# Kernel tuning notes

Measured on AMD Instinct MI355X. Metric: run time of the kernel, lower is better.

## Reference

```python
import jax, jax.numpy as jnp
import numpy as np

B, H = 16384, 64          # batch, human_num
SELF_DIM, HUMAN_DIM = 6, 7
D = 32                    # gcn2_w1_dim / embedding dim


def _lin(key, fin, fout):
    return jax.random.normal(key, (fin, fout), jnp.float32) / np.sqrt(fin)


def setup_inputs() -> dict:
    key = jax.random.key(0)
    ks = jax.random.split(key, 40)
    inp = {}
    inp["state"] = jax.random.normal(ks[0], (B, H, SELF_DIM + HUMAN_DIM), jnp.float32)
    inp["dropout"] = 0
    # w_r: mlp(6 -> 64 -> 32, last_relu=True)
    inp["wr_w1"] = _lin(ks[1], SELF_DIM, 64); inp["wr_b1"] = jnp.zeros(64, jnp.float32)
    inp["wr_w2"] = _lin(ks[2], 64, D);        inp["wr_b2"] = jnp.zeros(D, jnp.float32)
    # w_h: mlp(7 -> 64 -> 32, last_relu=True)
    inp["wh_w1"] = _lin(ks[3], HUMAN_DIM, 64); inp["wh_b1"] = jnp.zeros(64, jnp.float32)
    inp["wh_w2"] = _lin(ks[4], 64, D);         inp["wh_b2"] = jnp.zeros(D, jnp.float32)
    # hetero GraphConv weights: per edge type (rh: robot->human, hr: human->robot, hh: human->human),
    # per layer. GraphConv: out = lin_rel(scatter_sum(x_src)) + lin_root(x_dst); lin_root has no bias.
    i = 5
    for L in (1, 2):
        for et in ("rh", "hr", "hh"):
            inp[f"rel_{et}{L}"] = _lin(ks[i], D, D); i += 1
            inp[f"brel_{et}{L}"] = jnp.zeros(D, jnp.float32)
            inp[f"root_{et}{L}"] = _lin(ks[i], D, D); i += 1
    # value_net: mlp(32 -> 150 -> 100 -> 1), no last relu
    inp["vn_w1"] = _lin(ks[i], D, 150);  inp["vn_b1"] = jnp.zeros(150, jnp.float32); i += 1
    inp["vn_w2"] = _lin(ks[i], 150, 100); inp["vn_b2"] = jnp.zeros(100, jnp.float32); i += 1
    inp["vn_w3"] = _lin(ks[i], 100, 1);  inp["vn_b3"] = jnp.zeros(1, jnp.float32)
    return inp


def _hetero_layer(r, h, rel_rh, brel_rh, root_rh, rel_hr, brel_hr, root_hr,
                  rel_hh, brel_hh, root_hh):
    # r: [B, D] robot nodes; h: [B, H, D] human nodes
    sum_h = h.sum(axis=1)  # [B, D]
    # robot receives scatter-sum over all humans (star graph, one robot target)
    new_r = jax.nn.relu(sum_h @ rel_hr + brel_hr + r @ root_hr)
    # each human receives: robot message + sum of all OTHER humans (full graph minus self-loops)
    agg_hh = sum_h[:, None, :] - h  # [B, H, D]
    new_h = jax.nn.relu((r @ rel_rh)[:, None, :] + brel_rh
                        + agg_hh @ rel_hh + brel_hh
                        + h @ root_rh + h @ root_hh)
    return new_r, new_h


def _forward(state, wr_w1, wr_b1, wr_w2, wr_b2, wh_w1, wh_b1, wh_w2, wh_b2,
             rel_rh1, brel_rh1, root_rh1, rel_hr1, brel_hr1, root_hr1,
             rel_hh1, brel_hh1, root_hh1,
             rel_rh2, brel_rh2, root_rh2, rel_hr2, brel_hr2, root_hr2,
             rel_hh2, brel_hh2, root_hh2,
             vn_w1, vn_b1, vn_w2, vn_b2, vn_w3, vn_b3):
    self_state = state[:, 0, :SELF_DIM]        # [B, 6]
    human_states = state[:, :, SELF_DIM:]      # [B, H, 7]
    r = jax.nn.relu(jax.nn.relu(self_state @ wr_w1 + wr_b1) @ wr_w2 + wr_b2)      # [B, D]
    h = jax.nn.relu(jax.nn.relu(human_states @ wh_w1 + wh_b1) @ wh_w2 + wh_b2)    # [B, H, D]
    r, h = _hetero_layer(r, h, rel_rh1, brel_rh1, root_rh1, rel_hr1, brel_hr1,
                         root_hr1, rel_hh1, brel_hh1, root_hh1)
    r, h = _hetero_layer(r, h, rel_rh2, brel_rh2, root_rh2, rel_hr2, brel_hr2,
                         root_hr2, rel_hh2, brel_hh2, root_hh2)
    v = jax.nn.relu(r @ vn_w1 + vn_b1)
    v = jax.nn.relu(v @ vn_w2 + vn_b2)
    return v @ vn_w3 + vn_b3                    # [B, 1]


def reference(state, dropout, wr_w1, wr_b1, wr_w2, wr_b2, wh_w1, wh_b1, wh_w2, wh_b2,
              rel_rh1, brel_rh1, root_rh1, rel_hr1, brel_hr1, root_hr1,
              rel_hh1, brel_hh1, root_hh1,
              rel_rh2, brel_rh2, root_rh2, rel_hr2, brel_hr2, root_hr2,
              rel_hh2, brel_hh2, root_hh2,
              vn_w1, vn_b1, vn_w2, vn_b2, vn_w3, vn_b3):
    # dropout is accepted but unused (matches the torch forward signature)
    return _forward(state, wr_w1, wr_b1, wr_w2, wr_b2, wh_w1, wh_b1, wh_w2, wh_b2,
                    rel_rh1, brel_rh1, root_rh1, rel_hr1, brel_hr1, root_hr1,
                    rel_hh1, brel_hh1, root_hh1,
                    rel_rh2, brel_rh2, root_rh2, rel_hr2, brel_hr2, root_hr2,
                    rel_hh2, brel_hh2, root_hh2,
                    vn_w1, vn_b1, vn_w2, vn_b2, vn_w3, vn_b3)
```

## Files before the change

kernel.cpp:

```cpp
#include <hip/hip_runtime.h>

#define BTOT 16384

typedef __attribute__((ext_vector_type(8))) short bf16x8;
typedef __attribute__((ext_vector_type(4))) float f32x4;

#define MFMA16(a,b,c) __builtin_amdgcn_mfma_f32_16x16x32_bf16((a),(b),(c),0,0,0)

static __device__ __forceinline__ unsigned short bfhi(float x) {
    unsigned u = __float_as_uint(x);
    return (unsigned short)((u + 0x7FFFu + ((u >> 16) & 1u)) >> 16);
}
static __device__ __forceinline__ float b2f(unsigned short h) {
    return __uint_as_float(((unsigned)h) << 16);
}
static __device__ __forceinline__ unsigned short bflo(float x) {
    unsigned short h = bfhi(x);
    return bfhi(x - b2f(h));
}
static __device__ __forceinline__ unsigned pk2(float a, float b) {
    return (unsigned)bfhi(a) | ((unsigned)bfhi(b) << 16);
}
static __device__ __forceinline__ short f2s(float x) {
    return (short)bfhi(x);
}
static __device__ __forceinline__ bf16x8 zero8() {
    bf16x8 v;
    #pragma unroll
    for (int i = 0; i < 8; ++i) v[i] = 0;
    return v;
}

__global__ void pack_frags(
    const float* __restrict__ wh_w1, const float* __restrict__ wh_b1,
    const float* __restrict__ wh_w2,
    const float* __restrict__ root_rh1, const float* __restrict__ root_hh1,
    const float* __restrict__ rel_hh1,
    const float* __restrict__ wr_w2,
    const float* __restrict__ rel_hr1, const float* __restrict__ root_hr1,
    const float* __restrict__ rel_rh1,
    const float* __restrict__ rel_hr2, const float* __restrict__ root_hr2,
    const float* __restrict__ vn_w1, const float* __restrict__ vn_w2,
    const float* __restrict__ brel_hr1, const float* __restrict__ brel_rh1,
    const float* __restrict__ brel_hh1, const float* __restrict__ brel_hr2,
    short* __restrict__ pk)
{
    int t = blockIdx.x * blockDim.x + threadIdx.x;
    if (t < 52736) {
        int f = t >> 9, r = t & 511;
        int lane = r >> 3, j = r & 7;
        int q = lane >> 4, c = lane & 15;
        int k = q * 8 + j;
        unsigned short outv;
        if (f < 4) {
            int m = f * 16 + c;
            float v = (k < 7) ? wh_w1[k * 64 + m] : (k == 7 ? wh_b1[m] : 0.f);
            outv = bfhi(v);
        } else if (f < 8) {
            int u = f - 4, ks = u >> 1, nt = u & 1;
            outv = bfhi(wh_w2[(ks * 32 + k) * 32 + nt * 16 + c]);
        } else if (f < 10) {
            int n = (f - 8) * 16 + c;
            outv = bfhi(root_rh1[k * 32 + n] + root_hh1[k * 32 + n] - rel_hh1[k * 32 + n]);
        } else if (f < 22) {
            int u = f - 10, ks = u >> 1, nt = u & 1;
            int kp = ks * 32 + k;
            float w = wr_w2[(kp & 63) * 32 + nt * 16 + c];
            outv = (kp < 128) ? bfhi(w) : bflo(w);
        } else if (f < 46) {
            int u = f - 22, ks = u >> 2, nt = u & 3;
            int kp = ks * 32 + k, seg = kp >> 5, kk = kp & 31;
            int n2 = (nt & 1) * 16 + c;
            bool sPart = (seg < 2) || (seg == 4);
            const float* W = (nt < 2) ? (sPart ? rel_hr1 : root_hr1)
                                      : (sPart ? rel_hh1 : rel_rh1);
            float w = W[kk * 32 + n2];
            outv = (seg < 4) ? bfhi(w) : bflo(w);
        } else if (f < 58) {
            int u = f - 46, ks = u >> 1, nt = u & 1;
            int kp = ks * 32 + k, seg = kp >> 5, kk = kp & 31;
            int n = nt * 16 + c;
            bool sPart = (seg < 2) || (seg == 4);
            const float* W = sPart ? rel_hr2 : root_hr2;
            float w = W[kk * 32 + n];
            outv = (seg < 4) ? bfhi(w) : bflo(w);
        } else if (f < 68) {
            int n = (f - 58) * 16 + c;
            outv = (n < 150) ? bfhi(vn_w1[k * 150 + n]) : 0;
        } else {
            int u = f - 68, kt = u / 7, nt = u - kt * 7;
            int kk = kt * 32 + k, n = nt * 16 + c;
            outv = (kk < 150 && n < 100) ? bfhi(vn_w2[kk * 100 + n]) : 0;
        }
        pk[t] = (short)outv;
    } else if (t < 52800) {
        int i = t - 52736;
        float* bp = (float*)(pk + 52736);
        bp[i] = (i < 32) ? brel_hr1[i] : brel_rh1[i - 32] + brel_hh1[i - 32];
    } else if (t < 52832) {
        int i = t - 52800;
        float* bp = (float*)(pk + 52864);
        bp[i] = brel_hr2[i];
    }
}

__global__ __launch_bounds__(256) void fused_main(
    const float* __restrict__ state, const short* __restrict__ pk,
    const float* __restrict__ wr_w1, const float* __restrict__ wr_b1,
    const float* __restrict__ wr_b2, const float* __restrict__ wh_b2,
    short* __restrict__ r2buf)
{
    __shared__ short wbuf[4][4608];

    const int tid = threadIdx.x;
    const int wv = tid >> 6, lane = tid & 63;
    const int q = lane >> 4, c = lane & 15;
    const int b = blockIdx.x * 4 + wv;
    const float* st = state + (size_t)b * 832;
    short* T = wbuf[wv];

    const bf16x8* pk16 = (const bf16x8*)pk;
    const float* bg1f = (const float*)(pk + 52736);
    const float* bg2f = (const float*)(pk + 52864);
    const f32x4 z4 = {0.f, 0.f, 0.f, 0.f};

    bf16x8 A1[4], Bh2v[4], Bev[2];
    #pragma unroll
    for (int i = 0; i < 4; ++i) A1[i] = pk16[i * 64 + lane];
    #pragma unroll
    for (int i = 0; i < 4; ++i) Bh2v[i] = pk16[(4 + i) * 64 + lane];
    #pragma unroll
    for (int i = 0; i < 2; ++i) Bev[i] = pk16[(8 + i) * 64 + lane];

    {
        float hf[7];
        #pragma unroll
        for (int m = 0; m < 7; ++m) hf[m] = st[lane * 13 + 6 + m];
        uint4 v = make_uint4(pk2(hf[0], hf[1]), pk2(hf[2], hf[3]),
                             pk2(hf[4], hf[5]), pk2(hf[6], 1.0f));
        *(uint4*)(T + lane * 8) = v;
    }

    float trh;
    {
        float acc = wr_b1[lane];
        #pragma unroll
        for (int m = 0; m < 6; ++m) acc = fmaf(st[m], wr_w1[m * 64 + lane], acc);
        trh = fmaxf(acc, 0.f);
    }

    asm volatile("s_waitcnt lgkmcnt(0)" ::: "memory");

    bf16x8 bx[4];
    #pragma unroll
    for (int ht = 0; ht < 4; ++ht) {
        bf16x8 v = zero8();
        if (q == 0) v = *(const bf16x8*)(T + (ht * 16 + c) * 8);
        bx[ht] = v;
    }

    #pragma unroll
    for (int mh = 0; mh < 4; ++mh) {
        #pragma unroll
        for (int ht = 0; ht < 4; ++ht) {
            f32x4 d = MFMA16(A1[mh], bx[ht], z4);
            uint2 w = make_uint2(pk2(fmaxf(d[0], 0.f), fmaxf(d[1], 0.f)),
                                 pk2(fmaxf(d[2], 0.f), fmaxf(d[3], 0.f)));
            *(uint2*)(T + (ht * 16 + c) * 72 + mh * 16 + q * 4) = w;
        }
    }

    asm volatile("s_waitcnt lgkmcnt(0)" ::: "memory");

    const float b2a = wh_b2[c], b2b = wh_b2[16 + c];
    float ps0 = 0.f, ps1 = 0.f;
    #pragma unroll
    for (int mt = 0; mt < 4; ++mt) {
        bf16x8 a0 = *(const bf16x8*)(T + (mt * 16 + c) * 72 + q * 8);
        bf16x8 a1 = *(const bf16x8*)(T + (mt * 16 + c) * 72 + 32 + q * 8);
        f32x4 e0 = MFMA16(a0, Bh2v[0], z4); e0 = MFMA16(a1, Bh2v[2], e0);
        f32x4 e1 = MFMA16(a0, Bh2v[1], z4); e1 = MFMA16(a1, Bh2v[3], e1);
        #pragma unroll
        for (int r = 0; r < 4; ++r) {
            float v0 = fmaxf(e0[r] + b2a, 0.f), v1 = fmaxf(e1[r] + b2b, 0.f);
            int row = mt * 16 + q * 4 + r;
            T[row * 40 + c]      = f2s(v0);
            T[row * 40 + 16 + c] = f2s(v1);
            ps0 += v0; ps1 += v1;
        }
    }
    ps0 += __shfl_xor(ps0, 16); ps0 += __shfl_xor(ps0, 32);
    ps1 += __shfl_xor(ps1, 16); ps1 += __shfl_xor(ps1, 32);

    {
        short* SB = T + 2816;
        if (q == 0) {
            unsigned short h0 = bfhi(ps0), h1 = bfhi(ps1);
            SB[c] = (short)h0;        SB[16 + c] = (short)h1;
            SB[32 + c] = (short)bfhi(ps0 - b2f(h0));
            SB[48 + c] = (short)bfhi(ps1 - b2f(h1));
            SB[128 + c] = (short)h0;  SB[144 + c] = (short)h1;
        }
        short* TR = T + 3008;
        unsigned short th = bfhi(trh);
        TR[lane] = (short)th;
        TR[64 + lane] = (short)bfhi(trh - b2f(th));
        TR[128 + lane] = (short)th;
    }
    __syncthreads();

    if (wv == 0) {
        bf16x8 art[6];
        #pragma unroll
        for (int ks = 0; ks < 6; ++ks) {
            bf16x8 v = zero8();
            if (c < 4) v = *(const bf16x8*)(wbuf[c] + 3008 + ks * 32 + q * 8);
            art[ks] = v;
        }
        f32x4 dr0 = z4, dr1 = z4;
        #pragma unroll
        for (int ks = 0; ks < 6; ++ks) {
            dr0 = MFMA16(art[ks], pk16[(10 + ks * 2 + 0) * 64 + lane], dr0);
            dr1 = MFMA16(art[ks], pk16[(10 + ks * 2 + 1) * 64 + lane], dr1);
        }
        const float wb0 = wr_b2[c], wb1 = wr_b2[16 + c];
        if (q == 0) {
            #pragma unroll
            for (int r = 0; r < 4; ++r) {
                float v0 = fmaxf(dr0[r] + wb0, 0.f), v1 = fmaxf(dr1[r] + wb1, 0.f);
                short* SBr = wbuf[r] + 2816;
                unsigned short h0 = bfhi(v0), h1 = bfhi(v1);
                SBr[64 + c] = (short)h0;  SBr[96 + c]  = (short)bfhi(v0 - b2f(h0));  SBr[160 + c] = (short)h0;
                SBr[80 + c] = (short)h1;  SBr[112 + c] = (short)bfhi(v1 - b2f(h1));  SBr[176 + c] = (short)h1;
            }
        }
        asm volatile("s_waitcnt lgkmcnt(0)" ::: "memory");

        bf16x8 ag[6];
        #pragma unroll
        for (int ks = 0; ks < 6; ++ks) {
            bf16x8 v = zero8();
            if (c < 4) v = *(const bf16x8*)(wbuf[c] + 2816 + ks * 32 + q * 8);
            ag[ks] = v;
        }
        f32x4 dg[4] = {z4, z4, z4, z4};
        #pragma unroll
        for (int ks = 0; ks < 6; ++ks) {
            #pragma unroll
            for (int nt = 0; nt < 4; ++nt)
                dg[nt] = MFMA16(ag[ks], pk16[(22 + ks * 4 + nt) * 64 + lane], dg[nt]);
        }
        if (q == 0) {
            #pragma unroll
            for (int nt = 0; nt < 2; ++nt) {
                float bias = bg1f[nt * 16 + c];
                #pragma unroll
                for (int r = 0; r < 4; ++r) {
                    float v = fmaxf(dg[nt][r] + bias, 0.f);
                    short* G2r = wbuf[r] + 2624;
                    unsigned short hh = bfhi(v);
                    G2r[64 + nt * 16 + c]  = (short)hh;
                    G2r[96 + nt * 16 + c]  = (short)bfhi(v - b2f(hh));
                    G2r[160 + nt * 16 + c] = (short)hh;
                }
            }
            #pragma unroll
            for (int nt = 2; nt < 4; ++nt) {
                float bias = bg1f[nt * 16 + c];
                #pragma unroll
                for (int r = 0; r < 4; ++r)
                    ((float*)(wbuf[r] + 2560))[(nt - 2) * 16 + c] = dg[nt][r] + bias;
            }
        }
    }
    __syncthreads();

    {
        const float* C1 = (const float*)(T + 2560);
        const float c10 = C1[c], c11 = C1[16 + c];
        float t0 = 0.f, t1 = 0.f;
        #pragma unroll
        for (int mt = 0; mt < 4; ++mt) {
            bf16x8 ah = *(const bf16x8*)(T + (mt * 16 + c) * 40 + q * 8);
            f32x4 g0 = MFMA16(ah, Bev[0], z4);
            f32x4 g1 = MFMA16(ah, Bev[1], z4);
            #pragma unroll
            for (int r = 0; r < 4; ++r) {
                t0 += fmaxf(g0[r] + c10, 0.f);
                t1 += fmaxf(g1[r] + c11, 0.f);
            }
        }
        t0 += __shfl_xor(t0, 16); t0 += __shfl_xor(t0, 32);
        t1 += __shfl_xor(t1, 16); t1 += __shfl_xor(t1, 32);
        short* G2 = T + 2624;
        if (q == 0) {
            unsigned short h0 = bfhi(t0), h1 = bfhi(t1);
            G2[c] = (short)h0;        G2[16 + c] = (short)h1;
            G2[32 + c] = (short)bfhi(t0 - b2f(h0));
            G2[48 + c] = (short)bfhi(t1 - b2f(h1));
            G2[128 + c] = (short)h0;  G2[144 + c] = (short)h1;
        }
    }
    __syncthreads();

    if (wv == 0) {
        bf16x8 a2[6];
        #pragma unroll
        for (int ks = 0; ks < 6; ++ks) {
            bf16x8 v = zero8();
            if (c < 4) v = *(const bf16x8*)(wbuf[c] + 2624 + ks * 32 + q * 8);
            a2[ks] = v;
        }
        f32x4 d0 = z4, d1 = z4;
        #pragma unroll
        for (int ks = 0; ks < 6; ++ks) {
            d0 = MFMA16(a2[ks], pk16[(46 + ks * 2 + 0) * 64 + lane], d0);
            d1 = MFMA16(a2[ks], pk16[(46 + ks * 2 + 1) * 64 + lane], d1);
        }
        if (q == 0) {
            const int b0 = blockIdx.x * 4;
            const float g0 = bg2f[c], g1 = bg2f[16 + c];
            #pragma unroll
            for (int r = 0; r < 4; ++r) {
                r2buf[(b0 + r) * 32 + c]      = f2s(fmaxf(d0[r] + g0, 0.f));
                r2buf[(b0 + r) * 32 + 16 + c] = f2s(fmaxf(d1[r] + g1, 0.f));
            }
        }
    }
}

__global__ __launch_bounds__(256) void head_kernel(
    const short* __restrict__ pk,
    const float* __restrict__ vn_b1, const float* __restrict__ vn_b2,
    const float* __restrict__ vn_w3, const float* __restrict__ vn_b3,
    float* __restrict__ out)
{
    __shared__ __align__(16) short sh_v1[4][16 * 168];
    const int wv = threadIdx.x >> 6, lane = threadIdx.x & 63;
    const int q = lane >> 4, c = lane & 15;
    const int tile = blockIdx.x * 4 + wv;
    const bf16x8* wf = (const bf16x8*)pk;
    const short* r2b = pk + 53248;
    const f32x4 z4 = {0.f, 0.f, 0.f, 0.f};

    bf16x8 a1 = *(const bf16x8*)&r2b[(tile * 16 + c) * 32 + q * 8];
    short* vb = sh_v1[wv];
    #pragma unroll
    for (int nt = 0; nt < 10; ++nt) {
        f32x4 d = MFMA16(a1, wf[(58 + nt) * 64 + lane], z4);
        int n = nt * 16 + c;
        float bias = (n < 150) ? vn_b1[n] : 0.f;
        #pragma unroll
        for (int r = 0; r < 4; ++r) {
            float v = (n < 150) ? fmaxf(d[r] + bias, 0.f) : 0.f;
            vb[(q * 4 + r) * 168 + n] = f2s(v);
        }
    }
    __syncthreads();

    bf16x8 a2[5];
    #pragma unroll
    for (int kt = 0; kt < 5; ++kt)
        a2[kt] = *(const bf16x8*)&vb[c * 168 + kt * 32 + q * 8];

    float racc[4] = {0.f, 0.f, 0.f, 0.f};
    #pragma unroll
    for (int nt = 0; nt < 7; ++nt) {
        f32x4 d = z4;
        #pragma unroll
        for (int kt = 0; kt < 5; ++kt)
            d = MFMA16(a2[kt], wf[(68 + kt * 7 + nt) * 64 + lane], d);
        int n = nt * 16 + c;
        float bias = (n < 100) ? vn_b2[n] : 0.f;
        float w3   = (n < 100) ? vn_w3[n] : 0.f;
        #pragma unroll
        for (int r = 0; r < 4; ++r) racc[r] += fmaxf(d[r] + bias, 0.f) * w3;
    }
    #pragma unroll
    for (int m = 1; m < 16; m <<= 1) {
        #pragma unroll
        for (int r = 0; r < 4; ++r) racc[r] += __shfl_xor(racc[r], m);
    }
    if (c == 0) {
        float b3 = vn_b3[0];
        #pragma unroll
        for (int r = 0; r < 4; ++r) out[tile * 16 + q * 4 + r] = racc[r] + b3;
    }
}

extern "C" void kernel_launch(void* const* d_in, const int* in_sizes, int n_in,
                              void* d_out, int out_size, void* d_ws, size_t ws_size,
                              hipStream_t stream) {
    const float* state    = (const float*)d_in[0];
    const float* wr_w1    = (const float*)d_in[2];
    const float* wr_b1    = (const float*)d_in[3];
    const float* wr_w2    = (const float*)d_in[4];
    const float* wr_b2    = (const float*)d_in[5];
    const float* wh_w1    = (const float*)d_in[6];
    const float* wh_b1    = (const float*)d_in[7];
    const float* wh_w2    = (const float*)d_in[8];
    const float* wh_b2    = (const float*)d_in[9];
    const float* rel_rh1  = (const float*)d_in[10];
    const float* brel_rh1 = (const float*)d_in[11];
    const float* root_rh1 = (const float*)d_in[12];
    const float* rel_hr1  = (const float*)d_in[13];
    const float* brel_hr1 = (const float*)d_in[14];
    const float* root_hr1 = (const float*)d_in[15];
    const float* rel_hh1  = (const float*)d_in[16];
    const float* brel_hh1 = (const float*)d_in[17];
    const float* root_hh1 = (const float*)d_in[18];
    const float* rel_hr2  = (const float*)d_in[22];
    const float* brel_hr2 = (const float*)d_in[23];
    const float* root_hr2 = (const float*)d_in[24];
    const float* vn_w1    = (const float*)d_in[28];
    const float* vn_b1    = (const float*)d_in[29];
    const float* vn_w2    = (const float*)d_in[30];
    const float* vn_b2    = (const float*)d_in[31];
    const float* vn_w3    = (const float*)d_in[32];
    const float* vn_b3    = (const float*)d_in[33];
    float* out = (float*)d_out;
    short* pk  = (short*)d_ws;
    short* r2buf = pk + 53248;

    pack_frags<<<207, 256, 0, stream>>>(wh_w1, wh_b1, wh_w2,
                                        root_rh1, root_hh1, rel_hh1, wr_w2,
                                        rel_hr1, root_hr1, rel_rh1,
                                        rel_hr2, root_hr2, vn_w1, vn_w2,
                                        brel_hr1, brel_rh1, brel_hh1, brel_hr2, pk);
    fused_main<<<BTOT / 4, 256, 0, stream>>>(state, pk, wr_w1, wr_b1, wr_b2, wh_b2, r2buf);
    head_kernel<<<BTOT / 64, 256, 0, stream>>>(pk, vn_b1, vn_b2, vn_w3, vn_b3, out);
}
```

Baseline: 187.0 us.

## Swizzle LDS staging layouts and use hardware packed bf16 conversion

Replaces the padded LDS row layouts (strides 72 and 40) with XOR-swizzled unpadded layouts (strides 64 and 32) for the hidden and embedding tiles. Adds a matching permutation of the k index in the packed root weight fragment and relocates the other scratch offsets. The intent is to avoid LDS bank conflicts with less shared memory, and to write packed 32-bit pairs instead of separate 16-bit stores. It also switches the device-side bf16 rounding to the hardware cvt_pk_bf16_f32 builtin when available, keeping the software rounding for weight packing. The swizzle must agree exactly between writers and readers, including the k permutation, or results will be wrong.

```diff
diff --git a/kernel.cpp b/kernel.cpp
--- a/kernel.cpp
+++ b/kernel.cpp
@@ -7,22 +7,34 @@
 
 #define MFMA16(a,b,c) __builtin_amdgcn_mfma_f32_16x16x32_bf16((a),(b),(c),0,0,0)
 
+#if __has_builtin(__builtin_amdgcn_cvt_pk_bf16_f32)
+typedef __attribute__((ext_vector_type(2))) __bf16 hwbf2;
+static __device__ __forceinline__ unsigned pk2(float a, float b) {
+    hwbf2 v = __builtin_amdgcn_cvt_pk_bf16_f32(a, b);
+    return __builtin_bit_cast(unsigned, v);
+}
+#else
+static __device__ __forceinline__ unsigned pk2(float a, float b) {
+    unsigned ua = __float_as_uint(a), ub = __float_as_uint(b);
+    unsigned ra = (ua + 0x7FFFu + ((ua >> 16) & 1u)) >> 16;
+    unsigned rb = (ub + 0x7FFFu + ((ub >> 16) & 1u)) >> 16;
+    return (ra & 0xFFFFu) | (rb << 16);
+}
+#endif
 static __device__ __forceinline__ unsigned short bfhi(float x) {
+    return (unsigned short)(pk2(x, 0.f) & 0xFFFFu);
+}
+static __device__ __forceinline__ float b2f(unsigned short h) {
+    return __uint_as_float(((unsigned)h) << 16);
+}
+static __device__ __forceinline__ short f2s(float x) { return (short)bfhi(x); }
+static __device__ __forceinline__ unsigned short bfhi_m(float x) {
     unsigned u = __float_as_uint(x);
     return (unsigned short)((u + 0x7FFFu + ((u >> 16) & 1u)) >> 16);
 }
-static __device__ __forceinline__ float b2f(unsigned short h) {
-    return __uint_as_float(((unsigned)h) << 16);
-}
-static __device__ __forceinline__ unsigned short bflo(float x) {
-    unsigned short h = bfhi(x);
-    return bfhi(x - b2f(h));
-}
-static __device__ __forceinline__ unsigned pk2(float a, float b) {
-    return (unsigned)bfhi(a) | ((unsigned)bfhi(b) << 16);
-}
-static __device__ __forceinline__ short f2s(float x) {
-    return (short)bfhi(x);
+static __device__ __forceinline__ unsigned short bflo_m(float x) {
+    unsigned short h = bfhi_m(x);
+    return bfhi_m(x - b2f(h));
 }
 static __device__ __forceinline__ bf16x8 zero8() {
     bf16x8 v;
@@ -55,18 +67,19 @@
         if (f < 4) {
             int m = f * 16 + c;
             float v = (k < 7) ? wh_w1[k * 64 + m] : (k == 7 ? wh_b1[m] : 0.f);
-            outv = bfhi(v);
+            outv = bfhi_m(v);
         } else if (f < 8) {
             int u = f - 4, ks = u >> 1, nt = u & 1;
-            outv = bfhi(wh_w2[(ks * 32 + k) * 32 + nt * 16 + c]);
+            outv = bfhi_m(wh_w2[(ks * 32 + k) * 32 + nt * 16 + c]);
         } else if (f < 10) {
             int n = (f - 8) * 16 + c;
-            outv = bfhi(root_rh1[k * 32 + n] + root_hh1[k * 32 + n] - rel_hh1[k * 32 + n]);
+            int ko = (k >> 1) + ((k & 1) << 4);
+            outv = bfhi_m(root_rh1[ko * 32 + n] + root_hh1[ko * 32 + n] - rel_hh1[ko * 32 + n]);
         } else if (f < 22) {
             int u = f - 10, ks = u >> 1, nt = u & 1;
             int kp = ks * 32 + k;
             float w = wr_w2[(kp & 63) * 32 + nt * 16 + c];
-            outv = (kp < 128) ? bfhi(w) : bflo(w);
+            outv = (kp < 128) ? bfhi_m(w) : bflo_m(w);
         } else if (f < 46) {
             int u = f - 22, ks = u >> 2, nt = u & 3;
             int kp = ks * 32 + k, seg = kp >> 5, kk = kp & 31;
@@ -75,7 +88,7 @@
             const float* W = (nt < 2) ? (sPart ? rel_hr1 : root_hr1)
                                       : (sPart ? rel_hh1 : rel_rh1);
             float w = W[kk * 32 + n2];
-            outv = (seg < 4) ? bfhi(w) : bflo(w);
+            outv = (seg < 4) ? bfhi_m(w) : bflo_m(w);
         } else if (f < 58) {
             int u = f - 46, ks = u >> 1, nt = u & 1;
             int kp = ks * 32 + k, seg = kp >> 5, kk = kp & 31;
@@ -83,14 +96,14 @@
             bool sPart = (seg < 2) || (seg == 4);
             const float* W = sPart ? rel_hr2 : root_hr2;
             float w = W[kk * 32 + n];
-            outv = (seg < 4) ? bfhi(w) : bflo(w);
+            outv = (seg < 4) ? bfhi_m(w) : bflo_m(w);
         } else if (f < 68) {
             int n = (f - 58) * 16 + c;
-            outv = (n < 150) ? bfhi(vn_w1[k * 150 + n]) : 0;
+            outv = (n < 150) ? bfhi_m(vn_w1[k * 150 + n]) : 0;
         } else {
             int u = f - 68, kt = u / 7, nt = u - kt * 7;
             int kk = kt * 32 + k, n = nt * 16 + c;
-            outv = (kk < 150 && n < 100) ? bfhi(vn_w2[kk * 100 + n]) : 0;
+            outv = (kk < 150 && n < 100) ? bfhi_m(vn_w2[kk * 100 + n]) : 0;
         }
         pk[t] = (short)outv;
     } else if (t < 52800) {
@@ -110,7 +123,7 @@
     const float* __restrict__ wr_b2, const float* __restrict__ wh_b2,
     short* __restrict__ r2buf)
 {
-    __shared__ short wbuf[4][4608];
+    __shared__ short wbuf[4][4096];
 
     const int tid = threadIdx.x;
     const int wv = tid >> 6, lane = tid & 63;
@@ -166,7 +179,9 @@
             f32x4 d = MFMA16(A1[mh], bx[ht], z4);
             uint2 w = make_uint2(pk2(fmaxf(d[0], 0.f), fmaxf(d[1], 0.f)),
                                  pk2(fmaxf(d[2], 0.f), fmaxf(d[3], 0.f)));
-            *(uint2*)(T + (ht * 16 + c) * 72 + mh * 16 + q * 4) = w;
+            int row = ht * 16 + c;
+            int u = (2 * mh + (q >> 1)) ^ (c & 7);
+            *(uint2*)(T + row * 64 + u * 8 + (q & 1) * 4) = w;
         }
     }
 
@@ -176,16 +191,16 @@
     float ps0 = 0.f, ps1 = 0.f;
     #pragma unroll
     for (int mt = 0; mt < 4; ++mt) {
-        bf16x8 a0 = *(const bf16x8*)(T + (mt * 16 + c) * 72 + q * 8);
-        bf16x8 a1 = *(const bf16x8*)(T + (mt * 16 + c) * 72 + 32 + q * 8);
+        int row = mt * 16 + c;
+        bf16x8 a0 = *(const bf16x8*)(T + row * 64 + ((q ^ (c & 7))) * 8);
+        bf16x8 a1 = *(const bf16x8*)(T + row * 64 + (((q + 4) ^ (c & 7))) * 8);
         f32x4 e0 = MFMA16(a0, Bh2v[0], z4); e0 = MFMA16(a1, Bh2v[2], e0);
         f32x4 e1 = MFMA16(a0, Bh2v[1], z4); e1 = MFMA16(a1, Bh2v[3], e1);
         #pragma unroll
         for (int r = 0; r < 4; ++r) {
             float v0 = fmaxf(e0[r] + b2a, 0.f), v1 = fmaxf(e1[r] + b2b, 0.f);
-            int row = mt * 16 + q * 4 + r;
-            T[row * 40 + c]      = f2s(v0);
-            T[row * 40 + 16 + c] = f2s(v1);
+            int hrow = mt * 16 + q * 4 + r;
+            *(unsigned*)(T + hrow * 32 + (((c >> 2) ^ r)) * 8 + (c & 3) * 2) = pk2(v0, v1);
             ps0 += v0; ps1 += v1;
         }
     }
@@ -193,7 +208,7 @@
     ps1 += __shfl_xor(ps1, 16); ps1 += __shfl_xor(ps1, 32);
 
     {
-        short* SB = T + 2816;
+        short* SB = T + 3712;
         if (q == 0) {
             unsigned short h0 = bfhi(ps0), h1 = bfhi(ps1);
             SB[c] = (short)h0;        SB[16 + c] = (short)h1;
@@ -201,7 +216,7 @@
             SB[48 + c] = (short)bfhi(ps1 - b2f(h1));
             SB[128 + c] = (short)h0;  SB[144 + c] = (short)h1;
         }
-        short* TR = T + 3008;
+        short* TR = T + 3904;
         unsigned short th = bfhi(trh);
         TR[lane] = (short)th;
         TR[64 + lane] = (short)bfhi(trh - b2f(th));
@@ -214,7 +229,7 @@
         #pragma unroll
         for (int ks = 0; ks < 6; ++ks) {
             bf16x8 v = zero8();
-            if (c < 4) v = *(const bf16x8*)(wbuf[c] + 3008 + ks * 32 + q * 8);
+            if (c < 4) v = *(const bf16x8*)(wbuf[c] + 3904 + ks * 32 + q * 8);
             art[ks] = v;
         }
         f32x4 dr0 = z4, dr1 = z4;
@@ -228,7 +243,7 @@
             #pragma unroll
             for (int r = 0; r < 4; ++r) {
                 float v0 = fmaxf(dr0[r] + wb0, 0.f), v1 = fmaxf(dr1[r] + wb1, 0.f);
-                short* SBr = wbuf[r] + 2816;
+                short* SBr = wbuf[r] + 3712;
                 unsigned short h0 = bfhi(v0), h1 = bfhi(v1);
                 SBr[64 + c] = (short)h0;  SBr[96 + c]  = (short)bfhi(v0 - b2f(h0));  SBr[160 + c] = (short)h0;
                 SBr[80 + c] = (short)h1;  SBr[112 + c] = (short)bfhi(v1 - b2f(h1));  SBr[176 + c] = (short)h1;
@@ -240,7 +255,7 @@
         #pragma unroll
         for (int ks = 0; ks < 6; ++ks) {
             bf16x8 v = zero8();
-            if (c < 4) v = *(const bf16x8*)(wbuf[c] + 2816 + ks * 32 + q * 8);
+            if (c < 4) v = *(const bf16x8*)(wbuf[c] + 3712 + ks * 32 + q * 8);
             ag[ks] = v;
         }
         f32x4 dg[4] = {z4, z4, z4, z4};
@@ -257,7 +272,7 @@
                 #pragma unroll
                 for (int r = 0; r < 4; ++r) {
                     float v = fmaxf(dg[nt][r] + bias, 0.f);
-                    short* G2r = wbuf[r] + 2624;
+                    short* G2r = wbuf[r] + 3520;
                     unsigned short hh = bfhi(v);
                     G2r[64 + nt * 16 + c]  = (short)hh;
                     G2r[96 + nt * 16 + c]  = (short)bfhi(v - b2f(hh));
@@ -269,19 +284,20 @@
                 float bias = bg1f[nt * 16 + c];
                 #pragma unroll
                 for (int r = 0; r < 4; ++r)
-                    ((float*)(wbuf[r] + 2560))[(nt - 2) * 16 + c] = dg[nt][r] + bias;
+                    ((float*)(wbuf[r] + 3456))[(nt - 2) * 16 + c] = dg[nt][r] + bias;
             }
         }
     }
     __syncthreads();
 
     {
-        const float* C1 = (const float*)(T + 2560);
+        const float* C1 = (const float*)(T + 3456);
         const float c10 = C1[c], c11 = C1[16 + c];
         float t0 = 0.f, t1 = 0.f;
         #pragma unroll
         for (int mt = 0; mt < 4; ++mt) {
-            bf16x8 ah = *(const bf16x8*)(T + (mt * 16 + c) * 40 + q * 8);
+            int row = mt * 16 + c;
+            bf16x8 ah = *(const bf16x8*)(T + row * 32 + ((q ^ (c & 3))) * 8);
             f32x4 g0 = MFMA16(ah, Bev[0], z4);
             f32x4 g1 = MFMA16(ah, Bev[1], z4);
             #pragma unroll
@@ -292,7 +308,7 @@
         }
         t0 += __shfl_xor(t0, 16); t0 += __shfl_xor(t0, 32);
         t1 += __shfl_xor(t1, 16); t1 += __shfl_xor(t1, 32);
-        short* G2 = T + 2624;
+        short* G2 = T + 3520;
         if (q == 0) {
             unsigned short h0 = bfhi(t0), h1 = bfhi(t1);
             G2[c] = (short)h0;        G2[16 + c] = (short)h1;
@@ -308,7 +324,7 @@
         #pragma unroll
         for (int ks = 0; ks < 6; ++ks) {
             bf16x8 v = zero8();
-            if (c < 4) v = *(const bf16x8*)(wbuf[c] + 2624 + ks * 32 + q * 8);
+            if (c < 4) v = *(const bf16x8*)(wbuf[c] + 3520 + ks * 32 + q * 8);
             a2[ks] = v;
         }
         f32x4 d0 = z4, d1 = z4;
```

Result: no change. 183.7 us (-1.8%).
